# Performance work log

Hardware: AMD Instinct MI355X
Metric: run time of the kernel (lower is better)

The kernel has to match this reference:

```python
import jax, jax.numpy as jnp
import numpy as np

MAX_CACHE_LEN = 4096


def _rotate_half(t):
    d = t.shape[-1] // 2
    return jnp.concatenate([-t[..., d:], t[..., :d]], axis=-1)


def _apply_rope(t, cos, sin):
    # t: (B, S, H, D); cos/sin: (S, D)
    c = cos[None, :, None, :]
    s = sin[None, :, None, :]
    return t * c + _rotate_half(t) * s


def setup_inputs() -> dict:
    key = jax.random.key(0)
    ks = jax.random.split(key, 7)
    B, S, E, D, KVH = 1, 2048, 2048, 64, 8
    sc = 0.02
    x = jax.random.normal(ks[0], (B, S, E), dtype=jnp.float32)
    Wq = jax.random.normal(ks[1], (E, E), dtype=jnp.float32) * sc
    Wk = jax.random.normal(ks[2], (KVH * D, E), dtype=jnp.float32) * sc
    Wv = jax.random.normal(ks[3], (KVH * D, E), dtype=jnp.float32) * sc
    Wo = jax.random.normal(ks[4], (E, E), dtype=jnp.float32) * sc
    # RoPE tables
    pos = jnp.arange(S, dtype=jnp.float32)[:, None]
    inv_freq = 1.0 / (10000.0 ** (jnp.arange(0, D, 2, dtype=jnp.float32) / D))
    ang = pos * inv_freq[None, :]              # (S, D/2)
    ang = jnp.concatenate([ang, ang], axis=-1)  # (S, D)
    cos = jnp.cos(ang)
    sin = jnp.sin(ang)
    # additive causal mask (1,1,S,S): 0 where allowed, -1e9 where masked
    causal = jnp.tril(jnp.ones((S, S), dtype=bool))
    attn_mask = jnp.where(causal, 0.0, -1e9).astype(jnp.float32)[None, None]
    return {"x": x, "Wq": Wq, "Wk": Wk, "Wv": Wv, "Wo": Wo,
            "cos": cos, "sin": sin, "attn_mask": attn_mask, "last_pos": S}


def reference(x, Wq, Wk, Wv, Wo, cos, sin, attn_mask, last_pos):
    B, S, E = x.shape
    D = cos.shape[-1]
    H = E // D
    KVH = Wk.shape[0] // D
    group = H // KVH

    q = (x @ Wq.T).reshape(B, S, H, D)
    k = (x @ Wk.T).reshape(B, S, KVH, D)
    v = (x @ Wv.T).reshape(B, S, KVH, D)

    q = _apply_rope(q, cos, sin)
    k = _apply_rope(k, cos, sin)

    # KV-cache write (index_copy at positions [last_pos-S, last_pos)), then slice [:last_pos]
    key_cache = jnp.zeros((B, MAX_CACHE_LEN, KVH, D), dtype=x.dtype)
    value_cache = jnp.zeros((B, MAX_CACHE_LEN, KVH, D), dtype=x.dtype)
    key_cache = jax.lax.dynamic_update_slice(key_cache, jax.lax.stop_gradient(k), (0, last_pos - S, 0, 0))
    value_cache = jax.lax.dynamic_update_slice(value_cache, jax.lax.stop_gradient(v), (0, last_pos - S, 0, 0))
    kc = key_cache[:, :last_pos]    # (B, T, KVH, D)
    vc = value_cache[:, :last_pos]

    # GQA: repeat kv heads to match q heads
    kc = jnp.repeat(kc, group, axis=2)  # (B, T, H, D)
    vc = jnp.repeat(vc, group, axis=2)

    scale = 1.0 / np.sqrt(D)
    scores = jnp.einsum('bqhd,bkhd->bhqk', q, kc) * scale
    scores = scores + attn_mask
    probs = jax.nn.softmax(scores.astype(jnp.float32), axis=-1).astype(x.dtype)
    attn = jnp.einsum('bhqk,bkhd->bqhd', probs, vc)  # (B, S, H, D)
    out = attn.reshape(B, S, E) @ Wo.T
    return out
```

## Files before the change

kernel.cpp:

```cpp
#include <hip/hip_runtime.h>
#include <stdint.h>

typedef unsigned short u16;
typedef unsigned int   u32;

typedef __bf16 bf16x8 __attribute__((ext_vector_type(8)));
typedef float  fx4    __attribute__((ext_vector_type(4)));
typedef u16    u16x8  __attribute__((ext_vector_type(8)));

typedef __attribute__((address_space(1))) unsigned int as1_u32;
typedef __attribute__((address_space(3))) unsigned int as3_u32;

__device__ __forceinline__ void gload_lds16(const void* g, void* lds) {
  __builtin_amdgcn_global_load_lds((const as1_u32*)(uintptr_t)g,
                                   (as3_u32*)(uintptr_t)lds, 16, 0, 0);
}

__device__ __forceinline__ float b2f(u32 bits) {
  union { u32 i; float f; } v; v.i = bits << 16; return v.f;
}
__device__ __forceinline__ u16 f2b(float f) {
  union { float f; u32 i; } v; v.f = f;
  u32 x = v.i;
  return (u16)((x + 0x7fffu + ((x >> 16) & 1u)) >> 16);
}

__global__ __launch_bounds__(256) void cast_kernel(
    const float* __restrict__ s0, const float* __restrict__ s1,
    const float* __restrict__ s2, const float* __restrict__ s3,
    const float* __restrict__ s4, u16* __restrict__ dst)
{
  const size_t i8 = ((size_t)blockIdx.x * 256 + threadIdx.x) * 8;
  if (i8 >= 14680064) return;
  const float* src; size_t off;
  if      (i8 <  4194304) { src = s0; off = i8; }
  else if (i8 <  8388608) { src = s1; off = i8 - 4194304; }
  else if (i8 <  9437184) { src = s2; off = i8 - 8388608; }
  else if (i8 < 10485760) { src = s3; off = i8 - 9437184; }
  else                    { src = s4; off = i8 - 10485760; }
  const float4 a = *(const float4*)(src + off);
  const float4 b = *(const float4*)(src + off + 4);
  u16x8 o;
  o[0] = f2b(a.x); o[1] = f2b(a.y); o[2] = f2b(a.z); o[3] = f2b(a.w);
  o[4] = f2b(b.x); o[5] = f2b(b.y); o[6] = f2b(b.z); o[7] = f2b(b.w);
  *(u16x8*)(dst + i8) = o;
}

template <int MODE>
__global__ __launch_bounds__(256) void gemm_bt(
    const u16* __restrict__ A, const u16* __restrict__ B0,
    const u16* __restrict__ B1, const u16* __restrict__ B2,
    void* __restrict__ Cv, int K, int split1, int split2, int ldc,
    const float* __restrict__ cosb, const float* __restrict__ sinb)
{
  __shared__ __align__(16) u16 smem[4 * 128 * 32];

  const int n0 = blockIdx.x * 128;
  const int m0 = blockIdx.y * 128;

  const u16* Bsel; int nb;
  if (n0 < split1)      { Bsel = B0; nb = n0; }
  else if (n0 < split2) { Bsel = B1; nb = n0 - split1; }
  else                  { Bsel = B2; nb = n0 - split2; }

  const int tid  = threadIdx.x;
  const int wave = tid >> 6, lane = tid & 63;
  const int wm = wave >> 1, wn = wave & 1;
  const int quad = lane >> 4, l16 = lane & 15;

  fx4 acc[4][4];
#pragma unroll
  for (int i = 0; i < 4; ++i)
#pragma unroll
    for (int j = 0; j < 4; ++j) acc[i][j] = fx4{0.f, 0.f, 0.f, 0.f};

  auto stage = [&](int k0, int b) {
    u16* As = smem + b * 8192;
    u16* Bs = As + 4096;
#pragma unroll
    for (int i = 0; i < 2; ++i) {
      const int s   = tid + i * 256;
      const int row = s >> 2;
      const int c   = (s & 3) * 8;
      gload_lds16(A    + (size_t)(m0 + row) * K + k0 + c, As + s * 8);
      gload_lds16(Bsel + (size_t)(nb + row) * K + k0 + c, Bs + s * 8);
    }
  };

  const int KT = K >> 5;
  stage(0, 0);

#pragma unroll 1
  for (int kt = 0; kt < KT; ++kt) {
    const int cur = kt & 1;
    __syncthreads();
    if (kt + 1 < KT) stage((kt + 1) * 32, cur ^ 1);

    const u16* As = smem + cur * 8192;
    const u16* Bs = As + 4096;
    bf16x8 af[4], bfr[4];
#pragma unroll
    for (int t = 0; t < 4; ++t) {
      af[t]  = *(const bf16x8*)&As[(wm * 64 + t * 16 + l16) * 32 + quad * 8];
      bfr[t] = *(const bf16x8*)&Bs[(wn * 64 + t * 16 + l16) * 32 + quad * 8];
    }
#pragma unroll
    for (int ti = 0; ti < 4; ++ti)
#pragma unroll
      for (int tj = 0; tj < 4; ++tj)
        acc[ti][tj] = __builtin_amdgcn_mfma_f32_16x16x32_bf16(
            af[ti], bfr[tj], acc[ti][tj], 0, 0, 0);
  }

  if (MODE == 1) {
    float* C = (float*)Cv;
#pragma unroll
    for (int ti = 0; ti < 4; ++ti) {
      const int row_b = m0 + wm * 64 + ti * 16 + quad * 4;
#pragma unroll
      for (int tj = 0; tj < 4; ++tj) {
        const int col = n0 + wn * 64 + tj * 16 + l16;
#pragma unroll
        for (int r = 0; r < 4; ++r)
          C[(size_t)(row_b + r) * ldc + col] = acc[ti][tj][r];
      }
    }
  } else {
    u16* C = (u16*)Cv;
    const int cb = n0 + wn * 64;
    if (cb < 2560) {
      const float qs = (cb < 2048) ? 0.125f : 1.0f;
#pragma unroll
      for (int ti = 0; ti < 4; ++ti) {
#pragma unroll
        for (int r = 0; r < 4; ++r) {
          const int s = m0 + wm * 64 + ti * 16 + quad * 4 + r;
          const float* cr = cosb + s * 64;
          const float* sr = sinb + s * 64;
          u16* orow = C + (size_t)s * 3072 + cb;
#pragma unroll
          for (int tj = 0; tj < 2; ++tj) {
            const int d0 = tj * 16 + l16, d1 = d0 + 32;
            const float x0 = acc[ti][tj][r], x1 = acc[ti][tj + 2][r];
            orow[d0] = f2b((x0 * cr[d0] - x1 * sr[d0]) * qs);
            orow[d1] = f2b((x1 * cr[d1] + x0 * sr[d1]) * qs);
          }
        }
      }
    } else {
#pragma unroll
      for (int ti = 0; ti < 4; ++ti) {
        const int row_b = m0 + wm * 64 + ti * 16 + quad * 4;
#pragma unroll
        for (int tj = 0; tj < 4; ++tj) {
          const int col = cb + tj * 16 + l16;
#pragma unroll
          for (int r = 0; r < 4; ++r)
            C[(size_t)(row_b + r) * 3072 + col] = f2b(acc[ti][tj][r]);
        }
      }
    }
  }
}

__global__ __launch_bounds__(256) void vtrans_kernel(
    const u16* __restrict__ qkv, u16* __restrict__ vt)
{
  const int k0  = blockIdx.x * 64;
  const int kvh = blockIdx.y;
  const int vcol = 2560 + kvh * 64;
  __shared__ u16 T[64][72];
  const int tid = threadIdx.x;
#pragma unroll
  for (int i = 0; i < 2; ++i) {
    const int idx = tid + i * 256;
    const int j = idx >> 3, dc = (idx & 7) * 8;
    *(uint4*)&T[j][dc] = *(const uint4*)(qkv + (size_t)(k0 + j) * 3072 + vcol + dc);
  }
  __syncthreads();
#pragma unroll
  for (int i = 0; i < 2; ++i) {
    const int idx = tid + i * 256;
    const int d = idx >> 3, kg = (idx & 7) * 8;
    u16x8 o;
#pragma unroll
    for (int t = 0; t < 8; ++t) o[t] = T[kg + t][d];
    *(u16x8*)(vt + (size_t)(kvh * 64 + d) * 2048 + k0 + kg) = o;
  }
}

__global__ __launch_bounds__(256) void attn_kernel(
    const u16* __restrict__ qkv, const u16* __restrict__ vt,
    u16* __restrict__ attnbuf)
{
  const int h   = blockIdx.y;
  const int kvh = h >> 2;
  const int tid = threadIdx.x;
  const int w = tid >> 6, lane = tid & 63;
  const int quad = lane >> 4, l16 = lane & 15;

  __shared__ __align__(16) u16 Qs[64][72];
  __shared__ __align__(16) u16 Ks[64][72];
  __shared__ __align__(16) u16 Vt[64][72];
  __shared__ __align__(16) u16 Ps[4][16][72];

  const int kcol = 2048 + kvh * 64;

#pragma unroll 1
  for (int pass = 0; pass < 2; ++pass) {
    const int bx = pass ? (31 - blockIdx.x) : blockIdx.x;
    const int r0 = bx * 64;
    const int ntiles = bx + 1;

    __syncthreads();

#pragma unroll
    for (int i = 0; i < 2; ++i) {
      const int idx = tid + i * 256;
      const int r = idx >> 3, dc = (idx & 7) * 8;
      *(uint4*)&Qs[r][dc] = *(const uint4*)(qkv + (size_t)(r0 + r) * 3072 + h * 64 + dc);
    }

    fx4 O[4];
    float l_r[4];
#pragma unroll
    for (int c = 0; c < 4; ++c) O[c] = fx4{0.f, 0.f, 0.f, 0.f};
#pragma unroll
    for (int r = 0; r < 4; ++r) l_r[r] = 0.f;

    for (int kt = 0; kt < ntiles; ++kt) {
      const int k0 = kt * 64;
      __syncthreads();
#pragma unroll
      for (int i = 0; i < 2; ++i) {
        const int idx = tid + i * 256;
        const int j = idx >> 3, dc = (idx & 7) * 8;
        *(uint4*)&Ks[j][dc] = *(const uint4*)(qkv + (size_t)(k0 + j) * 3072 + kcol + dc);
        *(uint4*)&Vt[j][dc] = *(const uint4*)(vt + (size_t)(kvh * 64 + j) * 2048 + k0 + dc);
      }
      __syncthreads();

      const bf16x8 aq0 = *(const bf16x8*)&Qs[w * 16 + l16][quad * 8];
      const bf16x8 aq1 = *(const bf16x8*)&Qs[w * 16 + l16][32 + quad * 8];
      fx4 sc[4];
#pragma unroll
      for (int c = 0; c < 4; ++c) {
        const bf16x8 b0 = *(const bf16x8*)&Ks[c * 16 + l16][quad * 8];
        const bf16x8 b1 = *(const bf16x8*)&Ks[c * 16 + l16][32 + quad * 8];
        fx4 z = fx4{0.f, 0.f, 0.f, 0.f};
        z     = __builtin_amdgcn_mfma_f32_16x16x32_bf16(aq0, b0, z, 0, 0, 0);
        sc[c] = __builtin_amdgcn_mfma_f32_16x16x32_bf16(aq1, b1, z, 0, 0, 0);
      }

      const bool diag = (kt == ntiles - 1);
#pragma unroll
      for (int c = 0; c < 4; ++c) {
#pragma unroll
        for (int r = 0; r < 4; ++r) {
          float p = __expf(sc[c][r]);
          if (diag && (k0 + c * 16 + l16 > r0 + w * 16 + quad * 4 + r)) p = 0.f;
          l_r[r] += p;
          Ps[w][quad * 4 + r][c * 16 + l16] = f2b(p);
        }
      }

      const bf16x8 ap0 = *(const bf16x8*)&Ps[w][l16][quad * 8];
      const bf16x8 ap1 = *(const bf16x8*)&Ps[w][l16][32 + quad * 8];
#pragma unroll
      for (int c = 0; c < 4; ++c) {
        const bf16x8 v0 = *(const bf16x8*)&Vt[c * 16 + l16][quad * 8];
        const bf16x8 v1 = *(const bf16x8*)&Vt[c * 16 + l16][32 + quad * 8];
        O[c] = __builtin_amdgcn_mfma_f32_16x16x32_bf16(ap0, v0, O[c], 0, 0, 0);
        O[c] = __builtin_amdgcn_mfma_f32_16x16x32_bf16(ap1, v1, O[c], 0, 0, 0);
      }
    }

#pragma unroll
    for (int r = 0; r < 4; ++r) {
      float l = l_r[r];
#pragma unroll
      for (int off = 1; off < 16; off <<= 1) l += __shfl_xor(l, off, 64);
      const float inv = 1.f / fmaxf(l, 1e-30f);
      const int qg = r0 + w * 16 + quad * 4 + r;
#pragma unroll
      for (int c = 0; c < 4; ++c)
        attnbuf[(size_t)qg * 2048 + h * 64 + c * 16 + l16] = f2b(O[c][r] * inv);
    }
  }
}

extern "C" void kernel_launch(void* const* d_in, const int* in_sizes, int n_in,
                              void* d_out, int out_size, void* d_ws, size_t ws_size,
                              hipStream_t stream) {
  const float* x    = (const float*)d_in[0];
  const float* Wq   = (const float*)d_in[1];
  const float* Wk   = (const float*)d_in[2];
  const float* Wv   = (const float*)d_in[3];
  const float* Wo   = (const float*)d_in[4];
  const float* cosb = (const float*)d_in[5];
  const float* sinb = (const float*)d_in[6];
  float* out = (float*)d_out;

  u16* ws      = (u16*)d_ws;
  u16* qkv     = ws;
  u16* attnbuf = ws + 6291456;
  u16* xb      = ws + 10485760;
  u16* Wqb     = ws + 14680064;
  u16* Wkb     = ws + 18874368;
  u16* Wvb     = ws + 19922944;
  u16* Wob     = ws + 20971520;
  u16* vtg     = ws + 25165824;

  cast_kernel<<<7168, 256, 0, stream>>>(x, Wq, Wk, Wv, Wo, xb);

  gemm_bt<0><<<dim3(24, 16), 256, 0, stream>>>(
      xb, Wqb, Wkb, Wvb, qkv, 2048, 2048, 2560, 3072, cosb, sinb);

  vtrans_kernel<<<dim3(32, 8), 256, 0, stream>>>(qkv, vtg);

  attn_kernel<<<dim3(16, 32), 256, 0, stream>>>(qkv, vtg, attnbuf);

  gemm_bt<1><<<dim3(16, 16), 256, 0, stream>>>(
      attnbuf, Wob, Wob, Wob, out, 2048, 1 << 30, 1 << 30, 2048, cosb, sinb);
}
```

Measured before the change: 241.8 us.

## Triple-buffer GEMM loads, fuse V transpose into QKV epilogue, prefetch attention tiles

The GEMM moves from a double-buffered to a triple-buffered global-to-LDS pipeline, using explicit vmcnt waits in place of a full __syncthreads, so loads stay two stages ahead. The QKV GEMM epilogue now writes V straight into the transposed layout, which removes the separate vtrans kernel launch and its extra pass over V. The attention kernel prefetches the next K/V tile into registers while the current one is computed. The trade-offs are more LDS per block, more live registers, and V stores that scatter along the sequence dimension in small chunks.

```diff
diff --git a/kernel.cpp b/kernel.cpp
--- a/kernel.cpp
+++ b/kernel.cpp
@@ -7,6 +7,7 @@
 typedef __bf16 bf16x8 __attribute__((ext_vector_type(8)));
 typedef float  fx4    __attribute__((ext_vector_type(4)));
 typedef u16    u16x8  __attribute__((ext_vector_type(8)));
+typedef u16    u16x4  __attribute__((ext_vector_type(4)));
 
 typedef __attribute__((address_space(1))) unsigned int as1_u32;
 typedef __attribute__((address_space(3))) unsigned int as3_u32;
@@ -51,9 +52,10 @@
     const u16* __restrict__ A, const u16* __restrict__ B0,
     const u16* __restrict__ B1, const u16* __restrict__ B2,
     void* __restrict__ Cv, int K, int split1, int split2, int ldc,
-    const float* __restrict__ cosb, const float* __restrict__ sinb)
+    const float* __restrict__ cosb, const float* __restrict__ sinb,
+    u16* __restrict__ vtg)
 {
-  __shared__ __align__(16) u16 smem[4 * 128 * 32];
+  __shared__ __align__(16) u16 smem[3 * 8192];
 
   const int n0 = blockIdx.x * 128;
   const int m0 = blockIdx.y * 128;
@@ -74,30 +76,39 @@
 #pragma unroll
     for (int j = 0; j < 4; ++j) acc[i][j] = fx4{0.f, 0.f, 0.f, 0.f};
 
-  auto stage = [&](int k0, int b) {
+  const int row = tid >> 2;
+  const int cc  = (tid & 3) * 8;
+  auto stage = [&](int kt, int b) {
     u16* As = smem + b * 8192;
     u16* Bs = As + 4096;
+    const int k0 = kt * 32;
 #pragma unroll
     for (int i = 0; i < 2; ++i) {
-      const int s   = tid + i * 256;
-      const int row = s >> 2;
-      const int c   = (s & 3) * 8;
-      gload_lds16(A    + (size_t)(m0 + row) * K + k0 + c, As + s * 8);
-      gload_lds16(Bsel + (size_t)(nb + row) * K + k0 + c, Bs + s * 8);
+      const int r2 = row + i * 64;
+      const int s  = tid + i * 256;
+      gload_lds16(A    + (size_t)(m0 + r2) * K + k0 + cc, As + s * 8);
+      gload_lds16(Bsel + (size_t)(nb + r2) * K + k0 + cc, Bs + s * 8);
     }
   };
 
   const int KT = K >> 5;
   stage(0, 0);
-
+  stage(1, 1);
+
+  int cur = 0, nxt2 = 2;
 #pragma unroll 1
   for (int kt = 0; kt < KT; ++kt) {
-    const int cur = kt & 1;
-    __syncthreads();
-    if (kt + 1 < KT) stage((kt + 1) * 32, cur ^ 1);
+    if (kt < KT - 1) asm volatile("s_waitcnt vmcnt(4)\n\ts_barrier" ::: "memory");
+    else             asm volatile("s_waitcnt vmcnt(0)\n\ts_barrier" ::: "memory");
+    if (kt + 2 < KT) {
+      stage(kt + 2, nxt2);
+      nxt2 = (nxt2 == 2) ? 0 : nxt2 + 1;
+    }
 
     const u16* As = smem + cur * 8192;
     const u16* Bs = As + 4096;
+    cur = (cur == 2) ? 0 : cur + 1;
+
     bf16x8 af[4], bfr[4];
 #pragma unroll
     for (int t = 0; t < 4; ++t) {
@@ -148,44 +159,20 @@
         }
       }
     } else {
+      const int vr0 = cb - 2560;
 #pragma unroll
       for (int ti = 0; ti < 4; ++ti) {
-        const int row_b = m0 + wm * 64 + ti * 16 + quad * 4;
+        const int s0 = m0 + wm * 64 + ti * 16 + quad * 4;
 #pragma unroll
         for (int tj = 0; tj < 4; ++tj) {
-          const int col = cb + tj * 16 + l16;
-#pragma unroll
-          for (int r = 0; r < 4; ++r)
-            C[(size_t)(row_b + r) * 3072 + col] = f2b(acc[ti][tj][r]);
+          const int vr = vr0 + tj * 16 + l16;
+          u16x4 o;
+#pragma unroll
+          for (int r = 0; r < 4; ++r) o[r] = f2b(acc[ti][tj][r]);
+          *(u16x4*)(vtg + (size_t)vr * 2048 + s0) = o;
         }
       }
     }
-  }
-}
-
-__global__ __launch_bounds__(256) void vtrans_kernel(
-    const u16* __restrict__ qkv, u16* __restrict__ vt)
-{
-  const int k0  = blockIdx.x * 64;
-  const int kvh = blockIdx.y;
-  const int vcol = 2560 + kvh * 64;
-  __shared__ u16 T[64][72];
-  const int tid = threadIdx.x;
-#pragma unroll
-  for (int i = 0; i < 2; ++i) {
-    const int idx = tid + i * 256;
-    const int j = idx >> 3, dc = (idx & 7) * 8;
-    *(uint4*)&T[j][dc] = *(const uint4*)(qkv + (size_t)(k0 + j) * 3072 + vcol + dc);
-  }
-  __syncthreads();
-#pragma unroll
-  for (int i = 0; i < 2; ++i) {
-    const int idx = tid + i * 256;
-    const int d = idx >> 3, kg = (idx & 7) * 8;
-    u16x8 o;
-#pragma unroll
-    for (int t = 0; t < 8; ++t) o[t] = T[kg + t][d];
-    *(u16x8*)(vt + (size_t)(kvh * 64 + d) * 2048 + k0 + kg) = o;
   }
 }
 
@@ -205,6 +192,18 @@
   __shared__ __align__(16) u16 Ps[4][16][72];
 
   const int kcol = 2048 + kvh * 64;
+  const int sj = tid >> 3, sdc = (tid & 7) * 8;
+
+  uint4 pk[2], pv[2];
+  auto ldtile = [&](int kt) {
+    const int k0 = kt * 64;
+#pragma unroll
+    for (int i = 0; i < 2; ++i) {
+      const int j = sj + i * 32;
+      pk[i] = *(const uint4*)(qkv + (size_t)(k0 + j) * 3072 + kcol + sdc);
+      pv[i] = *(const uint4*)(vt + (size_t)(kvh * 64 + j) * 2048 + k0 + sdc);
+    }
+  };
 
 #pragma unroll 1
   for (int pass = 0; pass < 2; ++pass) {
@@ -212,14 +211,15 @@
     const int r0 = bx * 64;
     const int ntiles = bx + 1;
 
-    __syncthreads();
+    asm volatile("s_barrier" ::: "memory");
 
 #pragma unroll
     for (int i = 0; i < 2; ++i) {
-      const int idx = tid + i * 256;
-      const int r = idx >> 3, dc = (idx & 7) * 8;
-      *(uint4*)&Qs[r][dc] = *(const uint4*)(qkv + (size_t)(r0 + r) * 3072 + h * 64 + dc);
-    }
+      const int r = sj + i * 32;
+      *(uint4*)&Qs[r][sdc] =
+          *(const uint4*)(qkv + (size_t)(r0 + r) * 3072 + h * 64 + sdc);
+    }
+    ldtile(0);
 
     fx4 O[4];
     float l_r[4];
@@ -228,17 +228,18 @@
 #pragma unroll
     for (int r = 0; r < 4; ++r) l_r[r] = 0.f;
 
+#pragma unroll 1
     for (int kt = 0; kt < ntiles; ++kt) {
       const int k0 = kt * 64;
-      __syncthreads();
+      asm volatile("s_barrier" ::: "memory");
 #pragma unroll
       for (int i = 0; i < 2; ++i) {
-        const int idx = tid + i * 256;
-        const int j = idx >> 3, dc = (idx & 7) * 8;
-        *(uint4*)&Ks[j][dc] = *(const uint4*)(qkv + (size_t)(k0 + j) * 3072 + kcol + dc);
-        *(uint4*)&Vt[j][dc] = *(const uint4*)(vt + (size_t)(kvh * 64 + j) * 2048 + k0 + dc);
-      }
-      __syncthreads();
+        const int j = sj + i * 32;
+        *(uint4*)&Ks[j][sdc] = pk[i];
+        *(uint4*)&Vt[j][sdc] = pv[i];
+      }
+      if (kt + 1 < ntiles) ldtile(kt + 1);
+      asm volatile("s_waitcnt lgkmcnt(0)\n\ts_barrier" ::: "memory");
 
       const bf16x8 aq0 = *(const bf16x8*)&Qs[w * 16 + l16][quad * 8];
       const bf16x8 aq1 = *(const bf16x8*)&Qs[w * 16 + l16][32 + quad * 8];
@@ -314,12 +315,10 @@
   cast_kernel<<<7168, 256, 0, stream>>>(x, Wq, Wk, Wv, Wo, xb);
 
   gemm_bt<0><<<dim3(24, 16), 256, 0, stream>>>(
-      xb, Wqb, Wkb, Wvb, qkv, 2048, 2048, 2560, 3072, cosb, sinb);
-
-  vtrans_kernel<<<dim3(32, 8), 256, 0, stream>>>(qkv, vtg);
+      xb, Wqb, Wkb, Wvb, qkv, 2048, 2048, 2560, 3072, cosb, sinb, vtg);
 
   attn_kernel<<<dim3(16, 32), 256, 0, stream>>>(qkv, vtg, attnbuf);
 
   gemm_bt<1><<<dim3(16, 16), 256, 0, stream>>>(
-      attnbuf, Wob, Wob, Wob, out, 2048, 1 << 30, 1 << 30, 2048, cosb, sinb);
-}
+      attnbuf, Wob, Wob, Wob, out, 2048, 1 << 30, 1 << 30, 2048, cosb, sinb, vtg);
+}
```

Measured after the change: 270.8 us. 12.0% more time.
